# Performance work log

Measured on AMD Instinct MI355X. Metric: run time of the kernel, lower is better.

Reference implementation:

```python
import jax, jax.numpy as jnp
import numpy as np

B, NI, D, P, R = 32, 1024, 1024, 1000, 3  # batch, patches, d_model, pool_size, agg rounds


def setup_inputs() -> dict:
    key = jax.random.key(0)
    ks = jax.random.split(key, 12)
    w = lambda k, shape: jax.random.normal(k, shape, jnp.float32) * 0.02
    return {
        "att_feats": jax.random.normal(ks[0], (B, NI, D), jnp.float32),
        "fc_feats": jax.random.normal(ks[1], (B, D), jnp.float32),
        "pool": jax.random.normal(ks[2], (P, D), jnp.float32),
        "W_agg": w(ks[3], (R, D, D)),          # stacked agg projections (no bias)
        "Wq": w(ks[4], (D, D)), "bq": jnp.zeros((D,), jnp.float32),
        "Wk": w(ks[5], (D, D)), "bk": jnp.zeros((D,), jnp.float32),
        "Wv": w(ks[6], (D, D)), "bv": jnp.zeros((D,), jnp.float32),
        "Wc": w(ks[7], (D, D)), "bc": jnp.zeros((D,), jnp.float32),
        "Wg": w(ks[8], (2 * D,)), "bg": jnp.asarray(-1.0, jnp.float32),  # gate bias init -1
        "residual_scale": jnp.asarray(0.1, jnp.float32),
    }


def reference(att_feats, fc_feats, pool, W_agg, Wq, bq, Wk, bk, Wv, bv, Wc, bc, Wg, bg, residual_scale):
    d = att_feats.shape[-1]
    scale = 1.0 / jnp.sqrt(jnp.asarray(d, att_feats.dtype))
    v_hat = fc_feats  # fc dim == d_model path

    # Aggregate attention: R rounds over normality pool, averaged (Eq. 4-6)
    q_all = jnp.einsum('bd,rod->rbo', v_hat, W_agg)            # [R,B,D]
    scores = jnp.einsum('rbo,po->rbp', q_all, pool) * scale    # [R,B,P]
    weights = jax.nn.softmax(scores, axis=-1)
    v_agg = jnp.einsum('rbp,pd->bd', weights, pool) / R        # [B,D]

    # Differentiate attention (Eq. 7-10)
    q = v_hat @ Wq.T + bq
    k = v_agg @ Wk.T + bk
    v = v_agg @ Wv.T + bv
    sim = jnp.sum(q * k, axis=-1, keepdims=True) * scale       # [B,1]
    v_common = jax.nn.sigmoid(sim) * v
    v_diff = jax.nn.relu((v_hat - v_common) @ Wc.T + bc)       # [B,D] (dropout = identity, eval)

    # Gated residual; split gate weight to avoid materializing the concat
    Wg1, Wg2 = Wg[:d], Wg[d:]
    g = jax.nn.sigmoid(att_feats @ Wg1 + (v_diff @ Wg2)[:, None] + bg)  # [B,NI]
    return att_feats + residual_scale * g[..., None] * v_diff[:, None, :]
```

## Files before the change

kernel.cpp:

```cpp
#include <hip/hip_runtime.h>

#define D 1024
#define B 32
#define NI 1024
#define PP 1000
#define R 3
#define SPLITS 8
#define VS 8
#define BK 32
#define KT (D / SPLITS / BK)
#define PAD 34

typedef float f32x4_t __attribute__((ext_vector_type(4)));

__device__ __forceinline__ void nt_store4(float* p, float4 v) {
    f32x4_t x = {v.x, v.y, v.z, v.w};
    __builtin_nontemporal_store(x, (f32x4_t*)p);
}

__device__ __forceinline__ float wred(float x) {
    #pragma unroll
    for (int off = 32; off; off >>= 1) x += __shfl_xor(x, off, 64);
    return x;
}
__device__ __forceinline__ float wmax(float x) {
    #pragma unroll
    for (int off = 32; off; off >>= 1) x = fmaxf(x, __shfl_xor(x, off, 64));
    return x;
}

template<int NXS>
__device__ __forceinline__ void gemm_core(
        const float* __restrict__ A, int mbase, int Mrows,
        const float* __restrict__ Xb, int xrstride, size_t xss,
        int kc0, float acc[4][4]) {
    __shared__ float Ws[128][PAD];
    __shared__ float Xs[32][PAD];
    const int t = threadIdx.x;
    const int ty = t >> 3, tx = t & 7;
    const int m0 = 4 * ty, b0 = 4 * tx;
    const int lrow = t >> 3, lq = t & 7;

    #pragma unroll
    for (int i = 0; i < 4; ++i)
        #pragma unroll
        for (int j = 0; j < 4; ++j) acc[i][j] = 0.f;

    for (int kt = 0; kt < KT; ++kt) {
        const int kc = kc0 + kt * BK;
        #pragma unroll
        for (int rr = 0; rr < 4; ++rr) {
            const int row = lrow + 32 * rr;
            float4 v = make_float4(0.f, 0.f, 0.f, 0.f);
            if (mbase + row < Mrows)
                v = *(const float4*)(A + (size_t)(mbase + row) * D + kc + 4 * lq);
            *(float2*)&Ws[row][4 * lq]     = make_float2(v.x, v.y);
            *(float2*)&Ws[row][4 * lq + 2] = make_float2(v.z, v.w);
        }
        {
            const float* xp = Xb + (size_t)lrow * xrstride + kc + 4 * lq;
            float4 v = *(const float4*)xp;
            #pragma unroll
            for (int s = 1; s < NXS; ++s) {
                float4 w = *(const float4*)(xp + (size_t)s * xss);
                v.x += w.x; v.y += w.y; v.z += w.z; v.w += w.w;
            }
            *(float2*)&Xs[lrow][4 * lq]     = make_float2(v.x, v.y);
            *(float2*)&Xs[lrow][4 * lq + 2] = make_float2(v.z, v.w);
        }
        __syncthreads();
        #pragma unroll
        for (int kp = 0; kp < 16; ++kp) {
            float2 wv[4], xv[4];
            #pragma unroll
            for (int i = 0; i < 4; ++i) wv[i] = *(const float2*)&Ws[m0 + i][2 * kp];
            #pragma unroll
            for (int j = 0; j < 4; ++j) xv[j] = *(const float2*)&Xs[b0 + j][2 * kp];
            #pragma unroll
            for (int i = 0; i < 4; ++i)
                #pragma unroll
                for (int j = 0; j < 4; ++j) {
                    acc[i][j] += wv[i].x * xv[j].x;
                    acc[i][j] += wv[i].y * xv[j].y;
                }
        }
        __syncthreads();
    }
}

__global__ __launch_bounds__(256) void gemm_k1(const float* __restrict__ Wagg,
        const float* __restrict__ fc, float* __restrict__ Cp) {
    const int mb = blockIdx.x, s = blockIdx.y;
    const int mbase = mb * 128;
    float acc[4][4];
    gemm_core<1>(Wagg, mbase, R * D, fc, D, 0, s * 128, acc);
    const int t = threadIdx.x, ty = t >> 3, tx = t & 7;
    const int m = mbase + 4 * ty;
    #pragma unroll
    for (int j = 0; j < 4; ++j) {
        float* cp = Cp + ((size_t)(s * B) + 4 * tx + j) * (R * D) + m;
        *(float4*)cp = make_float4(acc[0][j], acc[1][j], acc[2][j], acc[3][j]);
    }
}

__global__ __launch_bounds__(256) void gemm_k2(const float* __restrict__ pool,
        const float* __restrict__ qallp, float* __restrict__ Cp) {
    const int mb = blockIdx.x, s = blockIdx.y, r = blockIdx.z;
    const int mbase = mb * 128;
    float acc[4][4];
    gemm_core<SPLITS>(pool, mbase, PP, qallp + r * D, R * D, (size_t)B * R * D,
                      s * 128, acc);
    const int t = threadIdx.x, ty = t >> 3, tx = t & 7;
    const int m = mbase + 4 * ty;
    if (m >= PP) return;
    #pragma unroll
    for (int j = 0; j < 4; ++j) {
        float* cp = Cp + ((size_t)((s * R + r) * B) + 4 * tx + j) * D + m;
        *(float4*)cp = make_float4(acc[0][j], acc[1][j], acc[2][j], acc[3][j]);
    }
}

__global__ __launch_bounds__(256) void gemm_k5(const float* __restrict__ Wq,
        const float* __restrict__ Wk, const float* __restrict__ Wv,
        const float* __restrict__ fc, const float* __restrict__ vaggp,
        float* __restrict__ Cp) {
    const int mb = blockIdx.x, s = blockIdx.y, z = blockIdx.z;
    const int mbase = mb * 128;
    float acc[4][4];
    if (z == 0)
        gemm_core<1>(Wq, mbase, D, fc, D, 0, s * 128, acc);
    else
        gemm_core<VS>((z == 1) ? Wk : Wv, mbase, D, vaggp, D, (size_t)B * D,
                      s * 128, acc);
    const int t = threadIdx.x, ty = t >> 3, tx = t & 7;
    const int m = mbase + 4 * ty;
    #pragma unroll
    for (int j = 0; j < 4; ++j) {
        float* cp = Cp + ((size_t)((s * R + z) * B) + 4 * tx + j) * D + m;
        *(float4*)cp = make_float4(acc[0][j], acc[1][j], acc[2][j], acc[3][j]);
    }
}

__global__ __launch_bounds__(256) void gemm_k7(const float* __restrict__ Wc,
        const float* __restrict__ u, float* __restrict__ Cp) {
    const int mb = blockIdx.x, s = blockIdx.y;
    const int mbase = mb * 128;
    float acc[4][4];
    gemm_core<1>(Wc, mbase, D, u, D, 0, s * 128, acc);
    const int t = threadIdx.x, ty = t >> 3, tx = t & 7;
    const int m = mbase + 4 * ty;
    #pragma unroll
    for (int j = 0; j < 4; ++j) {
        float* cp = Cp + ((size_t)(s * B) + 4 * tx + j) * D + m;
        *(float4*)cp = make_float4(acc[0][j], acc[1][j], acc[2][j], acc[3][j]);
    }
}

__global__ __launch_bounds__(256) void k3_wbar(const float* __restrict__ scp,
        float* __restrict__ wbar) {
    const int b = blockIdx.x;
    const int t = threadIdx.x, w = t >> 6, lane = t & 63;
    __shared__ float red[8];
    float wb[4] = {0.f, 0.f, 0.f, 0.f};
    for (int r = 0; r < R; ++r) {
        float v[4];
        float mx = -1e30f;
        #pragma unroll
        for (int i = 0; i < 4; ++i) {
            const int p = t + 256 * i;
            float x = -1e30f;
            if (p < PP) {
                x = 0.f;
                #pragma unroll
                for (int s = 0; s < SPLITS; ++s)
                    x += scp[((size_t)((s * R + r) * B) + b) * D + p];
                x *= 0.03125f;
            }
            v[i] = x;
            mx = fmaxf(mx, x);
        }
        mx = wmax(mx);
        if (lane == 0) red[w] = mx;
        __syncthreads();
        mx = fmaxf(fmaxf(red[0], red[1]), fmaxf(red[2], red[3]));
        float e[4], sum = 0.f;
        #pragma unroll
        for (int i = 0; i < 4; ++i) {
            const int p = t + 256 * i;
            e[i] = (p < PP) ? __expf(v[i] - mx) : 0.f;
            sum += e[i];
        }
        sum = wred(sum);
        if (lane == 0) red[4 + w] = sum;
        __syncthreads();
        const float inv = 1.f / (red[4] + red[5] + red[6] + red[7]);
        #pragma unroll
        for (int i = 0; i < 4; ++i) wb[i] += e[i] * inv;
        __syncthreads();
    }
    #pragma unroll
    for (int i = 0; i < 4; ++i) {
        const int p = t + 256 * i;
        wbar[(size_t)b * 1024 + p] = wb[i] * (1.f / 3.f);
    }
}

__global__ __launch_bounds__(256) void k4_vagg(const float* __restrict__ wbar,
        const float* __restrict__ pool, float* __restrict__ vaggp) {
    const int db = blockIdx.x, ps = blockIdx.y;
    __shared__ float Ps[32][132];
    __shared__ float Wbt[32][36];
    const int t = threadIdx.x;
    const int ty = t >> 3, tx = t & 7;
    float acc[4][4];
    #pragma unroll
    for (int i = 0; i < 4; ++i)
        #pragma unroll
        for (int j = 0; j < 4; ++j) acc[i][j] = 0.f;

    for (int pt = 0; pt < 4; ++pt) {
        const int p0 = ps * 128 + pt * 32;
        {
            const int prow = t >> 5, qc = t & 31;
            #pragma unroll
            for (int rr = 0; rr < 4; ++rr) {
                const int pr = prow + 8 * rr;
                float4 v = make_float4(0.f, 0.f, 0.f, 0.f);
                if (p0 + pr < PP)
                    v = *(const float4*)(pool + (size_t)(p0 + pr) * D + db * 128 + 4 * qc);
                *(float4*)&Ps[pr][4 * qc] = v;
            }
        }
        {
            const int bb = t >> 3, q = t & 7;
            float4 v = *(const float4*)(wbar + (size_t)bb * 1024 + p0 + 4 * q);
            Wbt[4 * q + 0][bb] = v.x; Wbt[4 * q + 1][bb] = v.y;
            Wbt[4 * q + 2][bb] = v.z; Wbt[4 * q + 3][bb] = v.w;
        }
        __syncthreads();
        #pragma unroll
        for (int pg = 0; pg < 8; ++pg) {
            #pragma unroll
            for (int pp = 0; pp < 4; ++pp) {
                const int p = 4 * pg + pp;
                float4 xv = *(const float4*)&Ps[p][4 * ty];
                float4 wv = *(const float4*)&Wbt[p][4 * tx];
                const float xs[4] = {xv.x, xv.y, xv.z, xv.w};
                const float wsv[4] = {wv.x, wv.y, wv.z, wv.w};
                #pragma unroll
                for (int i = 0; i < 4; ++i)
                    #pragma unroll
                    for (int j = 0; j < 4; ++j)
                        acc[i][j] += xs[i] * wsv[j];
            }
        }
        __syncthreads();
    }
    const int dbase = db * 128 + 4 * ty;
    #pragma unroll
    for (int j = 0; j < 4; ++j) {
        float* op = vaggp + ((size_t)ps * B + 4 * tx + j) * D + dbase;
        *(float4*)op = make_float4(acc[0][j], acc[1][j], acc[2][j], acc[3][j]);
    }
}

__global__ __launch_bounds__(256) void k6_u(const float* __restrict__ qkvp,
        const float* __restrict__ bq, const float* __restrict__ bk,
        const float* __restrict__ bv, const float* __restrict__ vhat,
        float* __restrict__ u) {
    const int b = blockIdx.x;
    const int t = threadIdx.x, w = t >> 6, lane = t & 63;
    const int d = 4 * t;
    float4 qv = *(const float4*)(bq + d);
    float4 kv = *(const float4*)(bk + d);
    #pragma unroll
    for (int s = 0; s < SPLITS; ++s) {
        float4 a = *(const float4*)(qkvp + ((size_t)((s * R + 0) * B) + b) * D + d);
        float4 c = *(const float4*)(qkvp + ((size_t)((s * R + 1) * B) + b) * D + d);
        qv.x += a.x; qv.y += a.y; qv.z += a.z; qv.w += a.w;
        kv.x += c.x; kv.y += c.y; kv.z += c.z; kv.w += c.w;
    }
    float local = qv.x * kv.x + qv.y * kv.y + qv.z * kv.z + qv.w * kv.w;
    local = wred(local);
    __shared__ float red[4];
    if (lane == 0) red[w] = local;
    __syncthreads();
    const float sim = (red[0] + red[1] + red[2] + red[3]) * 0.03125f;
    const float sig = 1.f / (1.f + __expf(-sim));
    float4 vv = *(const float4*)(bv + d);
    #pragma unroll
    for (int s = 0; s < SPLITS; ++s) {
        float4 c = *(const float4*)(qkvp + ((size_t)((s * R + 2) * B) + b) * D + d);
        vv.x += c.x; vv.y += c.y; vv.z += c.z; vv.w += c.w;
    }
    const float4 vh = *(const float4*)(vhat + (size_t)b * D + d);
    float4 o;
    o.x = vh.x - sig * vv.x; o.y = vh.y - sig * vv.y;
    o.z = vh.z - sig * vv.z; o.w = vh.w - sig * vv.w;
    *(float4*)(u + (size_t)b * D + d) = o;
}

__global__ __launch_bounds__(256) void k8_cb(const float* __restrict__ vdp,
        const float* __restrict__ bc, const float* __restrict__ Wg,
        const float* __restrict__ bg, float* __restrict__ vdiff,
        float* __restrict__ cb) {
    const int b = blockIdx.x;
    const int t = threadIdx.x, w = t >> 6, lane = t & 63;
    const int d = 4 * t;
    float4 a = *(const float4*)(bc + d);
    #pragma unroll
    for (int s = 0; s < SPLITS; ++s) {
        float4 c = *(const float4*)(vdp + ((size_t)(s * B) + b) * D + d);
        a.x += c.x; a.y += c.y; a.z += c.z; a.w += c.w;
    }
    a.x = fmaxf(a.x, 0.f); a.y = fmaxf(a.y, 0.f);
    a.z = fmaxf(a.z, 0.f); a.w = fmaxf(a.w, 0.f);
    *(float4*)(vdiff + (size_t)b * D + d) = a;
    const float4 g2 = *(const float4*)(Wg + D + d);
    float local = a.x * g2.x + a.y * g2.y + a.z * g2.z + a.w * g2.w;
    local = wred(local);
    __shared__ float red[4];
    if (lane == 0) red[w] = local;
    __syncthreads();
    if (t == 0) cb[b] = red[0] + red[1] + red[2] + red[3] + bg[0];
}

__global__ __launch_bounds__(256, 4) void k9_main(const float* __restrict__ att,
        const float* __restrict__ Wg, const float* __restrict__ cb,
        const float* __restrict__ vdiff, const float* __restrict__ rs_p,
        float* __restrict__ out) {
    __shared__ float vds[1024];
    const int t = threadIdx.x;
    const int b = blockIdx.x >> 5;
    *(float4*)&vds[4 * t] = *(const float4*)(vdiff + (size_t)b * D + 4 * t);
    __syncthreads();
    const int w = t >> 6, lane = t & 63;
    float4 g[4];
    #pragma unroll
    for (int kk = 0; kk < 4; ++kk)
        g[kk] = *(const float4*)(Wg + 4 * lane + 256 * kk);
    const float rsv = rs_p[0];
    const float cbb = cb[b];
    const size_t row0 = (size_t)b * NI + (size_t)(blockIdx.x & 31) * 32 + w * 8;
    const float* ap = att + row0 * D;
    float* op = out + row0 * D;

    float4 cur[8], nxt[8];
    #pragma unroll
    for (int q = 0; q < 8; ++q)
        cur[q] = *(const float4*)(ap + (size_t)(q >> 2) * D + 4 * lane + 256 * (q & 3));

    #pragma unroll
    for (int it = 0; it < 4; ++it) {
        if (it < 3) {
            const float* apn = ap + (size_t)(2 * it + 2) * D;
            #pragma unroll
            for (int q = 0; q < 8; ++q)
                nxt[q] = *(const float4*)(apn + (size_t)(q >> 2) * D + 4 * lane + 256 * (q & 3));
        }
        float acc0 = 0.f, acc1 = 0.f;
        #pragma unroll
        for (int kk = 0; kk < 4; ++kk) {
            acc0 += cur[kk].x * g[kk].x + cur[kk].y * g[kk].y +
                    cur[kk].z * g[kk].z + cur[kk].w * g[kk].w;
            acc1 += cur[4 + kk].x * g[kk].x + cur[4 + kk].y * g[kk].y +
                    cur[4 + kk].z * g[kk].z + cur[4 + kk].w * g[kk].w;
        }
        #pragma unroll
        for (int off = 32; off; off >>= 1) {
            acc0 += __shfl_xor(acc0, off, 64);
            acc1 += __shfl_xor(acc1, off, 64);
        }
        const float grs0 = rsv / (1.f + __expf(-(acc0 + cbb)));
        const float grs1 = rsv / (1.f + __expf(-(acc1 + cbb)));
        float* op0 = op + (size_t)(2 * it) * D;
        #pragma unroll
        for (int kk = 0; kk < 4; ++kk) {
            const int col = 4 * lane + 256 * kk;
            const float4 vd = *(const float4*)&vds[col];
            float4 o0, o1;
            o0.x = cur[kk].x + grs0 * vd.x; o0.y = cur[kk].y + grs0 * vd.y;
            o0.z = cur[kk].z + grs0 * vd.z; o0.w = cur[kk].w + grs0 * vd.w;
            o1.x = cur[4 + kk].x + grs1 * vd.x; o1.y = cur[4 + kk].y + grs1 * vd.y;
            o1.z = cur[4 + kk].z + grs1 * vd.z; o1.w = cur[4 + kk].w + grs1 * vd.w;
            nt_store4(op0 + col, o0);
            nt_store4(op0 + D + col, o1);
        }
        if (it < 3) {
            #pragma unroll
            for (int q = 0; q < 8; ++q) cur[q] = nxt[q];
        }
    }
}

extern "C" void kernel_launch(void* const* d_in, const int* in_sizes, int n_in,
                              void* d_out, int out_size, void* d_ws, size_t ws_size,
                              hipStream_t stream) {
    const float* att  = (const float*)d_in[0];
    const float* fc   = (const float*)d_in[1];
    const float* pool = (const float*)d_in[2];
    const float* Wagg = (const float*)d_in[3];
    const float* Wq   = (const float*)d_in[4];
    const float* bq   = (const float*)d_in[5];
    const float* Wk   = (const float*)d_in[6];
    const float* bk   = (const float*)d_in[7];
    const float* Wv   = (const float*)d_in[8];
    const float* bv   = (const float*)d_in[9];
    const float* Wc   = (const float*)d_in[10];
    const float* bc   = (const float*)d_in[11];
    const float* Wg   = (const float*)d_in[12];
    const float* bg   = (const float*)d_in[13];
    const float* rs   = (const float*)d_in[14];
    float* out = (float*)d_out;

    float* ws = (float*)d_ws;
    float* qallp = ws;
    float* scp   = qallp + (size_t)SPLITS * B * R * D;
    float* wbar  = scp + (size_t)SPLITS * R * B * D;
    float* vaggp = wbar + (size_t)B * 1024;
    float* qkvp  = vaggp + (size_t)VS * B * D;
    float* ub    = qkvp + (size_t)SPLITS * R * B * D;
    float* vdp   = ub + (size_t)B * D;
    float* vdiff = vdp + (size_t)SPLITS * B * D;
    float* cbuf  = vdiff + (size_t)B * D;

    gemm_k1<<<dim3(24, SPLITS), 256, 0, stream>>>(Wagg, fc, qallp);
    gemm_k2<<<dim3(8, SPLITS, R), 256, 0, stream>>>(pool, qallp, scp);
    k3_wbar<<<B, 256, 0, stream>>>(scp, wbar);
    k4_vagg<<<dim3(8, VS), 256, 0, stream>>>(wbar, pool, vaggp);
    gemm_k5<<<dim3(8, SPLITS, R), 256, 0, stream>>>(Wq, Wk, Wv, fc, vaggp, qkvp);
    k6_u<<<B, 256, 0, stream>>>(qkvp, bq, bk, bv, fc, ub);
    gemm_k7<<<dim3(8, SPLITS), 256, 0, stream>>>(Wc, ub, vdp);
    k8_cb<<<B, 256, 0, stream>>>(vdp, bc, Wg, bg, vdiff, cbuf);
    k9_main<<<B * 32, 256, 0, stream>>>(att, Wg, cbuf, vdiff, rs, out);
}
```

Baseline: 130.5 us.

## Stage attention rows through LDS with fully coalesced loads and finer blocks

The main gated-residual kernel now has each block load 8 contiguous rows of att_feats into shared memory with fully linear, coalesced float4 loads. Each wave then reads its two rows back from LDS to compute the gate dot product and write the output. The grid grows from 1024 to 4096 blocks and the register double-buffering across iterations is removed, so latency hiding relies on occupancy instead. The 36 KB of LDS per block limits how many blocks fit per CU, and there is an extra LDS round trip.

```diff
diff --git a/kernel.cpp b/kernel.cpp
--- a/kernel.cpp
+++ b/kernel.cpp
@@ -325,71 +325,65 @@
     if (t == 0) cb[b] = red[0] + red[1] + red[2] + red[3] + bg[0];
 }
 
-__global__ __launch_bounds__(256, 4) void k9_main(const float* __restrict__ att,
+__global__ __launch_bounds__(256) void k9_main(const float* __restrict__ att,
         const float* __restrict__ Wg, const float* __restrict__ cb,
         const float* __restrict__ vdiff, const float* __restrict__ rs_p,
         float* __restrict__ out) {
+    __shared__ float atile[8 * 1024];
     __shared__ float vds[1024];
-    const int t = threadIdx.x;
-    const int b = blockIdx.x >> 5;
-    *(float4*)&vds[4 * t] = *(const float4*)(vdiff + (size_t)b * D + 4 * t);
-    __syncthreads();
-    const int w = t >> 6, lane = t & 63;
+    const int t = threadIdx.x, w = t >> 6, lane = t & 63;
+    const int b = blockIdx.x >> 7;
+    const size_t row0 = (size_t)blockIdx.x * 8;
+    const float* ap = att + row0 * D;
+
+    float4 st[8];
+    #pragma unroll
+    for (int i = 0; i < 8; ++i)
+        st[i] = *(const float4*)(ap + (i * 256 + t) * 4);
     float4 g[4];
     #pragma unroll
     for (int kk = 0; kk < 4; ++kk)
         g[kk] = *(const float4*)(Wg + 4 * lane + 256 * kk);
+    const float4 vdl = *(const float4*)(vdiff + (size_t)b * D + 4 * t);
     const float rsv = rs_p[0];
     const float cbb = cb[b];
-    const size_t row0 = (size_t)b * NI + (size_t)(blockIdx.x & 31) * 32 + w * 8;
-    const float* ap = att + row0 * D;
-    float* op = out + row0 * D;
-
-    float4 cur[8], nxt[8];
-    #pragma unroll
-    for (int q = 0; q < 8; ++q)
-        cur[q] = *(const float4*)(ap + (size_t)(q >> 2) * D + 4 * lane + 256 * (q & 3));
-
-    #pragma unroll
-    for (int it = 0; it < 4; ++it) {
-        if (it < 3) {
-            const float* apn = ap + (size_t)(2 * it + 2) * D;
-            #pragma unroll
-            for (int q = 0; q < 8; ++q)
-                nxt[q] = *(const float4*)(apn + (size_t)(q >> 2) * D + 4 * lane + 256 * (q & 3));
-        }
-        float acc0 = 0.f, acc1 = 0.f;
-        #pragma unroll
-        for (int kk = 0; kk < 4; ++kk) {
-            acc0 += cur[kk].x * g[kk].x + cur[kk].y * g[kk].y +
-                    cur[kk].z * g[kk].z + cur[kk].w * g[kk].w;
-            acc1 += cur[4 + kk].x * g[kk].x + cur[4 + kk].y * g[kk].y +
-                    cur[4 + kk].z * g[kk].z + cur[4 + kk].w * g[kk].w;
-        }
-        #pragma unroll
-        for (int off = 32; off; off >>= 1) {
-            acc0 += __shfl_xor(acc0, off, 64);
-            acc1 += __shfl_xor(acc1, off, 64);
-        }
-        const float grs0 = rsv / (1.f + __expf(-(acc0 + cbb)));
-        const float grs1 = rsv / (1.f + __expf(-(acc1 + cbb)));
-        float* op0 = op + (size_t)(2 * it) * D;
-        #pragma unroll
-        for (int kk = 0; kk < 4; ++kk) {
-            const int col = 4 * lane + 256 * kk;
-            const float4 vd = *(const float4*)&vds[col];
-            float4 o0, o1;
-            o0.x = cur[kk].x + grs0 * vd.x; o0.y = cur[kk].y + grs0 * vd.y;
-            o0.z = cur[kk].z + grs0 * vd.z; o0.w = cur[kk].w + grs0 * vd.w;
-            o1.x = cur[4 + kk].x + grs1 * vd.x; o1.y = cur[4 + kk].y + grs1 * vd.y;
-            o1.z = cur[4 + kk].z + grs1 * vd.z; o1.w = cur[4 + kk].w + grs1 * vd.w;
-            nt_store4(op0 + col, o0);
-            nt_store4(op0 + D + col, o1);
-        }
-        if (it < 3) {
-            #pragma unroll
-            for (int q = 0; q < 8; ++q) cur[q] = nxt[q];
-        }
+    #pragma unroll
+    for (int i = 0; i < 8; ++i)
+        *(float4*)&atile[(i * 256 + t) * 4] = st[i];
+    *(float4*)&vds[4 * t] = vdl;
+    __syncthreads();
+
+    const int r0 = 2 * w;
+    float acc0 = 0.f, acc1 = 0.f;
+    #pragma unroll
+    for (int kk = 0; kk < 4; ++kk) {
+        const int col = 4 * lane + 256 * kk;
+        const float4 a0 = *(const float4*)&atile[r0 * 1024 + col];
+        const float4 a1 = *(const float4*)&atile[(r0 + 1) * 1024 + col];
+        acc0 += a0.x * g[kk].x + a0.y * g[kk].y + a0.z * g[kk].z + a0.w * g[kk].w;
+        acc1 += a1.x * g[kk].x + a1.y * g[kk].y + a1.z * g[kk].z + a1.w * g[kk].w;
+    }
+    #pragma unroll
+    for (int off = 32; off; off >>= 1) {
+        acc0 += __shfl_xor(acc0, off, 64);
+        acc1 += __shfl_xor(acc1, off, 64);
+    }
+    const float grs0 = rsv / (1.f + __expf(-(acc0 + cbb)));
+    const float grs1 = rsv / (1.f + __expf(-(acc1 + cbb)));
+    float* op = out + (row0 + r0) * D;
+    #pragma unroll
+    for (int kk = 0; kk < 4; ++kk) {
+        const int col = 4 * lane + 256 * kk;
+        const float4 a0 = *(const float4*)&atile[r0 * 1024 + col];
+        const float4 a1 = *(const float4*)&atile[(r0 + 1) * 1024 + col];
+        const float4 vd = *(const float4*)&vds[col];
+        float4 o0, o1;
+        o0.x = a0.x + grs0 * vd.x; o0.y = a0.y + grs0 * vd.y;
+        o0.z = a0.z + grs0 * vd.z; o0.w = a0.w + grs0 * vd.w;
+        o1.x = a1.x + grs1 * vd.x; o1.y = a1.y + grs1 * vd.y;
+        o1.z = a1.z + grs1 * vd.z; o1.w = a1.w + grs1 * vd.w;
+        nt_store4(op + col, o0);
+        nt_store4(op + D + col, o1);
     }
 }
 
@@ -432,5 +426,5 @@
     k6_u<<<B, 256, 0, stream>>>(qkvp, bq, bk, bv, fc, ub);
     gemm_k7<<<dim3(8, SPLITS), 256, 0, stream>>>(Wc, ub, vdp);
     k8_cb<<<B, 256, 0, stream>>>(vdp, bc, Wg, bg, vdiff, cbuf);
-    k9_main<<<B * 32, 256, 0, stream>>>(att, Wg, cbuf, vdiff, rs, out);
-}
+    k9_main<<<B * NI / 8, 256, 0, stream>>>(att, Wg, cbuf, vdiff, rs, out);
+}
```

After: 130.0 us. About the same (-0.4%).
